# Optimization experiments

Measured on AMD Instinct MI355X. Metric: run time of the kernel, lower is better.

Reference implementation:

```python
import jax, jax.numpy as jnp
import numpy as np

EPS = 1e-12  # F.normalize default eps


def conv3d(x, w, b=None):
    # x: (B,C,D,H,W), w: (O,I,3,3,3), stride 1, padding 1 == SAME
    y = jax.lax.conv_general_dilated(
        x, w, window_strides=(1, 1, 1), padding='SAME',
        dimension_numbers=('NCDHW', 'OIDHW', 'NCDHW'))
    if b is not None:
        y = y + b[None, :, None, None, None]
    return y


def adaptive_conv(x, weights):
    # x: (B,C,D,H,W); weights: (B,27,D,H,W) per-voxel 3x3x3 kernel taps
    B, C, D, H, W = x.shape
    xp = jnp.pad(x, ((0, 0), (0, 0), (1, 1), (1, 1), (1, 1)))
    out = jnp.zeros_like(x)
    idx = 0
    for i in range(3):
        for j in range(3):
            for k in range(3):
                out = out + xp[:, :, i:i + D, j:j + H, k:k + W] * weights[:, idx][:, None]
                idx += 1
    return out


def adaptive_block(inputs, w1, b1, w2, weights_src=None):
    # weights = Conv3d(8->8) -> ReLU -> Conv3d(8->27, no bias), then L1-normalize over channel
    src = inputs if weights_src is None else weights_src
    w = conv3d(jax.nn.relu(conv3d(src, w1, b1)), w2)
    norm = jnp.maximum(jnp.sum(jnp.abs(w), axis=1, keepdims=True), EPS)
    w = w / norm
    out = inputs
    for _ in range(3):
        out = adaptive_conv(out, w)
    return out


def setup_inputs() -> dict:
    key = jax.random.key(0)
    ks = jax.random.split(key, 16)
    d = {}
    d['x'] = jax.random.normal(ks[0], (1, 8, 128, 128, 128), dtype=jnp.float32)
    s = 0.05
    d['ac1_w1'] = jax.random.normal(ks[1], (8, 8, 3, 3, 3), jnp.float32) * s
    d['ac1_b1'] = jnp.zeros((8,), jnp.float32)
    d['ac1_w2'] = jax.random.normal(ks[2], (27, 8, 3, 3, 3), jnp.float32) * s
    d['ac2_w1'] = jax.random.normal(ks[3], (8, 8, 3, 3, 3), jnp.float32) * s
    d['ac2_b1'] = jnp.zeros((8,), jnp.float32)
    d['ac2_w2'] = jax.random.normal(ks[4], (27, 8, 3, 3, 3), jnp.float32) * s
    d['ac3_w1'] = jax.random.normal(ks[5], (8, 8, 3, 3, 3), jnp.float32) * s
    d['ac3_b1'] = jnp.zeros((8,), jnp.float32)
    d['ac3_w2'] = jax.random.normal(ks[6], (27, 8, 3, 3, 3), jnp.float32) * s
    d['mid_w'] = jax.random.normal(ks[7], (8, 8, 3, 3, 3), jnp.float32) * s
    d['mid_b'] = jnp.zeros((8,), jnp.float32)
    d['out_w'] = jax.random.normal(ks[8], (1, 8, 3, 3, 3), jnp.float32) * s
    d['out_b'] = jnp.zeros((1,), jnp.float32)
    return d


def reference(x, ac1_w1, ac1_b1, ac1_w2, ac2_w1, ac2_b1, ac2_w2,
              ac3_w1, ac3_b1, ac3_w2, mid_w, mid_b, out_w, out_b):
    # Post-UNet refinement pipeline of Voxel_RefinerXL.run
    mid = adaptive_block(x, ac1_w1, ac1_b1, ac1_w2)
    mid = conv3d(mid, mid_w, mid_b)
    mid = adaptive_block(mid, ac2_w1, ac2_b1, ac2_w2)
    final = conv3d(mid, out_w, out_b)  # (B,1,D,H,W)
    final = adaptive_block(final, ac3_w1, ac3_b1, ac3_w2, weights_src=mid)
    return final
```

## Files before the change

kernel.cpp:

```cpp
#include <hip/hip_runtime.h>
#include <hip/hip_fp16.h>
#include <math.h>

#define WW 128
#define HH 128
#define DD 128
#define HW (WW * HH)
#define VOL (WW * HH * DD)
#define PW 130
#define PHW (130 * 130)
#define PVOL (130 * 130 * 130)
#define NSHELL 99848

typedef _Float16 f16x8 __attribute__((ext_vector_type(8)));
typedef _Float16 f16x4 __attribute__((ext_vector_type(4)));
typedef _Float16 f16x2 __attribute__((ext_vector_type(2)));
typedef float f32x4 __attribute__((ext_vector_type(4)));
typedef float f32x16 __attribute__((ext_vector_type(16)));
typedef int int4v __attribute__((ext_vector_type(4)));
typedef int int2v __attribute__((ext_vector_type(2)));

__device__ __forceinline__ void stv(float* p, float v) { *p = v; }
__device__ __forceinline__ void stv(_Float16* p, float v) { *p = (_Float16)v; }


template <int NCH>
__global__ __launch_bounds__(256) void zero_shell2(_Float16* __restrict__ p0,
                                                   _Float16* __restrict__ p1)
{
    _Float16* p = blockIdx.y ? p1 : p0;
    const int t = blockIdx.x * 256 + threadIdx.x;
    if (t >= NSHELL) return;
    int d, h, w;
    if (t < 33800)      { d = (t < 16900) ? 0 : 129; int r = t % 16900; h = r / 130; w = r % 130; }
    else if (t < 67080) { int r = t - 33800; h = (r < 16640) ? 0 : 129; int q = r % 16640; d = 1 + q / 130; w = q % 130; }
    else                { int r = t - 67080; w = (r < 16384) ? 0 : 129; int q = r % 16384; d = 1 + q / 128; h = 1 + q % 128; }
    const size_t site = (size_t)d * PHW + (size_t)h * PW + w;
    if (NCH == 8) *(f16x8*)(p + site * 8) = (f16x8){};
    else          p[site] = (_Float16)0.f;
}

__global__ __launch_bounds__(256) void cvt_x(const float* __restrict__ x,
                                             _Float16* __restrict__ xi)
{
    const size_t v = (size_t)blockIdx.x * 256 + threadIdx.x;
    const int d = (int)(v >> 14), h = (int)((v >> 7) & 127), w = (int)(v & 127);
    f16x8 o;
#pragma unroll
    for (int c = 0; c < 8; ++c) o[c] = (_Float16)x[(size_t)c * VOL + v];
    *(f16x8*)(xi + ((size_t)(d + 1) * PHW + (size_t)(h + 1) * PW + (w + 1)) * 8) = o;
}

__global__ __launch_bounds__(256) void prepack_all(
    const float* __restrict__ w0, const float* __restrict__ w1,
    const float* __restrict__ w2, const float* __restrict__ w3,
    const float* __restrict__ w4, const float* __restrict__ w5,
    const float* __restrict__ w6, const float* __restrict__ w7,
    _Float16* __restrict__ pb)
{
    const int b = blockIdx.x;
    const float* src; int OC; size_t off;
    switch (b) {
        case 0: src = w0; OC = 8;  off = 0;     break;
        case 1: src = w1; OC = 8;  off = 3584;  break;
        case 2: src = w2; OC = 8;  off = 7168;  break;
        case 3: src = w3; OC = 8;  off = 10752; break;
        case 4: src = w4; OC = 1;  off = 14336; break;
        case 5: src = w5; OC = 27; off = 17920; break;
        case 6: src = w6; OC = 27; off = 25088; break;
        default: src = w7; OC = 27; off = 32256; break;
    }
    const bool big = (b >= 5);
    const int total = big ? 896 : 448;
    for (int e = threadIdx.x; e < total; e += 256) {
        const int s = e >> 6, lane = e & 63;
        const int m   = big ? (lane & 31) : (lane & 15);
        const int tap = big ? (2 * s + (lane >> 5)) : (s * 4 + (lane >> 4));
        f16x8 a = {};
        if (tap < 27 && m < OC) {
#pragma unroll
            for (int j = 0; j < 8; ++j)
                a[j] = (_Float16)src[m * 216 + j * 27 + tap];
        }
        *(f16x8*)(pb + off + (size_t)e * 8) = a;
    }
}

template <int OC, bool RELU, int OM, typename TO>
__global__ __launch_bounds__(256) void conv_g(const _Float16* __restrict__ in,
                                              const _Float16* __restrict__ apack,
                                              const float* __restrict__ bias,
                                              TO* __restrict__ out)
{
    const int tid  = threadIdx.x;
    const int wid  = tid >> 6;
    const int lane = tid & 63;
    const int n    = lane & 15;
    const int quad = lane >> 4;

    const int bid = blockIdx.x;
    const int idx = bid >> 3;
    const int d   = ((bid & 7) << 4) + (idx & 15);
    const int h   = ((idx >> 4) << 2) + wid;

    f16x8 afr[7];
#pragma unroll
    for (int s = 0; s < 7; ++s)
        afr[s] = *(const f16x8*)(apack + (size_t)(s * 64 + lane) * 8);

    int voff[7];
#pragma unroll
    for (int s = 0; s < 7; ++s) {
        int tap = s * 4 + quad;
        if (tap > 26) tap = 26;
        const int kd = tap / 9, kh = (tap % 9) / 3, kw = tap % 3;
        voff[s] = (d + kd) * PHW + (h + kh) * PW + kw;
    }

    float bv[4];
#pragma unroll
    for (int r = 0; r < 4; ++r) {
        const int o = quad * 4 + r;
        bv[r] = (bias != nullptr && o < OC) ? bias[o] : 0.f;
    }

#pragma unroll 2
    for (int wseg = 0; wseg < 8; ++wseg) {
        const int wv = wseg * 16 + n;
        f16x8 bfr[7];
#pragma unroll
        for (int s = 0; s < 7; ++s)
            bfr[s] = *(const f16x8*)(in + (size_t)(voff[s] + wv) * 8);
        f32x4 acc;
        acc[0] = bv[0]; acc[1] = bv[1]; acc[2] = bv[2]; acc[3] = bv[3];
#pragma unroll
        for (int s = 0; s < 7; ++s)
            acc = __builtin_amdgcn_mfma_f32_16x16x32_f16(afr[s], bfr[s], acc, 0, 0, 0);

        if (OM == 0) {
            if (quad < 2) {
                const size_t pvox = (size_t)(d + 1) * PHW + (size_t)(h + 1) * PW + 1 + wv;
                f16x4 o4;
#pragma unroll
                for (int r = 0; r < 4; ++r) {
                    float v = acc[r];
                    if (RELU) v = fmaxf(v, 0.f);
                    o4[r] = (_Float16)v;
                }
                *(f16x4*)((_Float16*)out + pvox * 8 + quad * 4) = o4;
            }
        } else {
            if (quad == 0) {
                const size_t pvox = (size_t)(d + 1) * PHW + (size_t)(h + 1) * PW + 1 + wv;
                float v = acc[0];
                if (RELU) v = fmaxf(v, 0.f);
                stv((TO*)out + pvox, v);
            }
        }
    }
}

__global__ __launch_bounds__(256, 4) void conv27_g(const _Float16* __restrict__ in,
                                                   const _Float16* __restrict__ apack,
                                                   _Float16* __restrict__ wn)
{
    __shared__ f16x8 lds[2340];

    const int tid  = threadIdx.x;
    const int wid  = tid >> 6;
    const int lane = tid & 63;
    const int col  = lane & 31;
    const int half = lane >> 5;

    const int bid = blockIdx.x;
    const int idx = bid >> 3;
    const int d   = ((bid & 7) << 4) + (idx & 15);
    const int h0  = (idx >> 4) << 2;
    const int h   = h0 + wid;

    f16x8 sv[10];
#pragma unroll
    for (int it = 0; it < 10; ++it) {
        const int sidx = it * 256 + tid;
        if (sidx < 2340) {
            const int dd = sidx / 780;
            const int r  = sidx - dd * 780;
            const int hh = r / 130;
            const int ww = r - hh * 130;
            sv[it] = *(const f16x8*)(in + ((size_t)(d + dd) * PHW + (size_t)(h0 + hh) * PW + ww) * 8);
        }
    }
#pragma unroll
    for (int it = 0; it < 10; ++it) {
        const int sidx = it * 256 + tid;
        if (sidx < 2340) lds[sidx] = sv[it];
    }
    __syncthreads();

    f16x8 afr[14];
#pragma unroll
    for (int s = 0; s < 14; ++s)
        afr[s] = *(const f16x8*)(apack + (size_t)(s * 64 + lane) * 8);

    int vsite[14];
#pragma unroll
    for (int s = 0; s < 14; ++s) {
        int tap = 2 * s + half;
        if (tap > 26) tap = 26;
        const int kd = tap / 9, kh = (tap % 9) / 3, kw = tap % 3;
        vsite[s] = (kd * 6 + wid + kh) * 130 + kw + col;
    }

#pragma unroll 1
    for (int wseg = 0; wseg < 4; ++wseg) {
        const int wb = wseg * 32;
        f16x8 bfr[6];
#pragma unroll
        for (int s = 0; s < 6; ++s)
            bfr[s] = lds[vsite[s] + wb];
        f32x16 acc = {};
#pragma unroll
        for (int s = 0; s < 14; ++s) {
            acc = __builtin_amdgcn_mfma_f32_32x32x16_f16(afr[s], bfr[s % 6], acc, 0, 0, 0);
            if (s + 6 < 14)
                bfr[s % 6] = lds[vsite[s + 6] + wb];
        }

        float p0 = (fabsf(acc[0]) + fabsf(acc[1])) + (fabsf(acc[2]) + fabsf(acc[3]));
        float p1 = (fabsf(acc[4]) + fabsf(acc[5])) + (fabsf(acc[6]) + fabsf(acc[7]));
        float p2 = (fabsf(acc[8]) + fabsf(acc[9])) + (fabsf(acc[10]) + fabsf(acc[11]));
        float p3 = (fabsf(acc[12]) + fabsf(acc[13])) + (fabsf(acc[14]) + fabsf(acc[15]));
        float ssum = (p0 + p1) + (p2 + p3);
        ssum += __shfl_xor(ssum, 32);
        const float inv = __builtin_amdgcn_rcpf(fmaxf(ssum, 1e-12f));

        int pk[8];
#pragma unroll
        for (int i = 0; i < 8; ++i) {
            f16x2 t;
            t[0] = (_Float16)(acc[2 * i] * inv);
            t[1] = (_Float16)(acc[2 * i + 1] * inv);
            pk[i] = __builtin_bit_cast(int, t);
        }
        const size_t grp = (size_t)(d * 128 + h) * 4 + wseg;
        _Float16* gbase = wn + grp * 896;
        if (half == 0) {
            _Float16* dst = gbase + (size_t)col * 16;
            int4v v0; v0[0] = pk[0]; v0[1] = pk[1]; v0[2] = pk[2]; v0[3] = pk[3];
            int4v v1; v1[0] = pk[4]; v1[1] = pk[5]; v1[2] = pk[6]; v1[3] = pk[7];
            *(int4v*)dst = v0;
            *(int4v*)(dst + 8) = v1;
        } else {
            _Float16* dst = gbase + 512 + (size_t)col * 12;
            int2v a; a[0] = pk[0]; a[1] = pk[1];
            int2v b; b[0] = pk[2]; b[1] = pk[3];
            int2v c; c[0] = pk[4]; c[1] = pk[5];
            *(int2v*)dst = a;
            *(int2v*)(dst + 4) = b;
            *(int2v*)(dst + 8) = c;
        }
    }
}

#define WH(m) (((m) >> 2) & 1)
#define WR(m) (((m) & 3) + 4 * ((m) >> 3))

__global__ __launch_bounds__(256) void adapt8(const _Float16* __restrict__ in,
                                              const _Float16* __restrict__ wn,
                                              _Float16* __restrict__ out)
{
    const int tid = threadIdx.x;
    const int bid = blockIdx.x;
    const int d = bid >> 6;
    const int h = ((bid & 63) << 1) + (tid >> 7);
    const int w = tid & 127;
    const size_t vox = (size_t)d * HW + (size_t)h * WW + w;

    const _Float16* gb = wn + (vox >> 5) * 896;
    const int col = (int)(vox & 31);
    f16x8 wk0[2];
    wk0[0] = *(const f16x8*)(gb + (size_t)col * 16);
    wk0[1] = *(const f16x8*)(gb + (size_t)col * 16 + 8);
    f16x4 wk1[3];
    const _Float16* c1 = gb + 512 + (size_t)col * 12;
    wk1[0] = *(const f16x4*)(c1);
    wk1[1] = *(const f16x4*)(c1 + 4);
    wk1[2] = *(const f16x4*)(c1 + 8);

    float acc[8] = {0.f, 0.f, 0.f, 0.f, 0.f, 0.f, 0.f, 0.f};
#pragma unroll
    for (int kd = 0; kd < 3; ++kd) {
#pragma unroll
        for (int kh = 0; kh < 3; ++kh) {
            const _Float16* rp = in + ((size_t)(d + kd) * PHW + (size_t)(h + kh) * PW + w) * 8;
#pragma unroll
            for (int kw = 0; kw < 3; ++kw) {
                const f16x8 xv = *(const f16x8*)(rp + (size_t)kw * 8);
                const int m = kd * 9 + kh * 3 + kw;
                const int r = WR(m);
                const float wvv = WH(m) == 0 ? (float)wk0[r >> 3][r & 7]
                                             : (float)wk1[r >> 2][r & 3];
#pragma unroll
                for (int c = 0; c < 8; ++c) acc[c] += wvv * (float)xv[c];
            }
        }
    }
    f16x8 o;
#pragma unroll
    for (int c = 0; c < 8; ++c) o[c] = (_Float16)acc[c];
    *(f16x8*)(out + ((size_t)(d + 1) * PHW + (size_t)(h + 1) * PW + (w + 1)) * 8) = o;
}

template <bool PADOUT, typename TOUT>
__global__ __launch_bounds__(256) void adapt1(const _Float16* __restrict__ in,
                                              const _Float16* __restrict__ wn,
                                              TOUT* __restrict__ out)
{
    const size_t vox = (size_t)blockIdx.x * 256 + threadIdx.x;
    const int w = (int)(vox & 127);
    const int h = (int)((vox >> 7) & 127);
    const int d = (int)(vox >> 14);

    const _Float16* gb = wn + (vox >> 5) * 896;
    const int col = (int)(vox & 31);
    f16x8 wk0[2];
    wk0[0] = *(const f16x8*)(gb + (size_t)col * 16);
    wk0[1] = *(const f16x8*)(gb + (size_t)col * 16 + 8);
    f16x4 wk1[3];
    const _Float16* c1 = gb + 512 + (size_t)col * 12;
    wk1[0] = *(const f16x4*)(c1);
    wk1[1] = *(const f16x4*)(c1 + 4);
    wk1[2] = *(const f16x4*)(c1 + 8);

    float acc = 0.f;
#pragma unroll
    for (int kd = 0; kd < 3; ++kd) {
#pragma unroll
        for (int kh = 0; kh < 3; ++kh) {
            const _Float16* rp = in + (size_t)(d + kd) * PHW + (size_t)(h + kh) * PW + w;
#pragma unroll
            for (int kw = 0; kw < 3; ++kw) {
                const int m = kd * 9 + kh * 3 + kw;
                const int r = WR(m);
                const float wvv = WH(m) == 0 ? (float)wk0[r >> 3][r & 7]
                                             : (float)wk1[r >> 2][r & 3];
                acc += wvv * (float)rp[kw];
            }
        }
    }
    if (PADOUT)
        stv(out + (size_t)(d + 1) * PHW + (size_t)(h + 1) * PW + (w + 1), acc);
    else
        stv(out + vox, acc);
}

extern "C" void kernel_launch(void* const* d_in, const int* in_sizes, int n_in,
                              void* d_out, int out_size, void* d_ws, size_t ws_size,
                              hipStream_t stream)
{
    (void)in_sizes; (void)n_in; (void)out_size; (void)ws_size;

    const float* x      = (const float*)d_in[0];
    const float* ac1_w1 = (const float*)d_in[1];
    const float* ac1_b1 = (const float*)d_in[2];
    const float* ac1_w2 = (const float*)d_in[3];
    const float* ac2_w1 = (const float*)d_in[4];
    const float* ac2_b1 = (const float*)d_in[5];
    const float* ac2_w2 = (const float*)d_in[6];
    const float* ac3_w1 = (const float*)d_in[7];
    const float* ac3_b1 = (const float*)d_in[8];
    const float* ac3_w2 = (const float*)d_in[9];
    const float* mid_w  = (const float*)d_in[10];
    const float* mid_b  = (const float*)d_in[11];
    const float* out_w  = (const float*)d_in[12];
    const float* out_b  = (const float*)d_in[13];
    float* outp = (float*)d_out;

    const size_t V = (size_t)VOL;
    _Float16* Wb  = (_Float16*)d_ws;
    _Float16* B1i = Wb + 32 * V;
    _Float16* B2i = B1i + (size_t)8 * PVOL;
    _Float16* F0  = B2i + (size_t)8 * PVOL;
    _Float16* F1  = F0 + (size_t)PVOL;
    _Float16* PB  = F1 + (size_t)PVOL;

    _Float16* pk_ac1w1 = PB + 0;
    _Float16* pk_ac2w1 = PB + 3584;
    _Float16* pk_ac3w1 = PB + 7168;
    _Float16* pk_midw  = PB + 10752;
    _Float16* pk_outw  = PB + 14336;
    _Float16* pk_ac1w2 = PB + 17920;
    _Float16* pk_ac2w2 = PB + 25088;
    _Float16* pk_ac3w2 = PB + 32256;

    const dim3 cgrid(4096), cblk(256);
    const dim3 a8grid(8192), a8blk(256);
    const dim3 a1grid(8192), a1blk(256);
    const dim3 zgrid((NSHELL + 255) / 256, 2), zblk(256);

    zero_shell2<8><<<zgrid, zblk, 0, stream>>>(B1i, B2i);
    zero_shell2<1><<<zgrid, zblk, 0, stream>>>(F0, F1);
    prepack_all<<<8, 256, 0, stream>>>(ac1_w1, ac2_w1, ac3_w1, mid_w, out_w,
                                       ac1_w2, ac2_w2, ac3_w2, PB);
    cvt_x<<<8192, 256, 0, stream>>>(x, B2i);

    conv_g<8, true, 0, _Float16><<<cgrid, cblk, 0, stream>>>(B2i, pk_ac1w1, ac1_b1, B1i);
    conv27_g<<<cgrid, cblk, 0, stream>>>(B1i, pk_ac1w2, Wb);
    adapt8<<<a8grid, a8blk, 0, stream>>>(B2i, Wb, B1i);
    adapt8<<<a8grid, a8blk, 0, stream>>>(B1i, Wb, B2i);
    adapt8<<<a8grid, a8blk, 0, stream>>>(B2i, Wb, B1i);
    conv_g<8, false, 0, _Float16><<<cgrid, cblk, 0, stream>>>(B1i, pk_midw, mid_b, B2i);

    conv_g<8, true, 0, _Float16><<<cgrid, cblk, 0, stream>>>(B2i, pk_ac2w1, ac2_b1, B1i);
    conv27_g<<<cgrid, cblk, 0, stream>>>(B1i, pk_ac2w2, Wb);
    adapt8<<<a8grid, a8blk, 0, stream>>>(B2i, Wb, B1i);
    adapt8<<<a8grid, a8blk, 0, stream>>>(B1i, Wb, B2i);
    adapt8<<<a8grid, a8blk, 0, stream>>>(B2i, Wb, B1i);

    conv_g<8, true, 0, _Float16><<<cgrid, cblk, 0, stream>>>(B1i, pk_ac3w1, ac3_b1, B2i);
    conv27_g<<<cgrid, cblk, 0, stream>>>(B2i, pk_ac3w2, Wb);
    conv_g<1, false, 2, _Float16><<<cgrid, cblk, 0, stream>>>(B1i, pk_outw, out_b, F0);
    adapt1<true, _Float16><<<a1grid, a1blk, 0, stream>>>(F0, Wb, F1);
    adapt1<true, _Float16><<<a1grid, a1blk, 0, stream>>>(F1, Wb, F0);
    adapt1<false, float><<<a1grid, a1blk, 0, stream>>>(F0, Wb, outp);
}
```

Measured before the change: 734.9 us.

## Stage adaptive-conv input halo tiles in LDS with 4-row blocks

The adapt8 and adapt1 kernels now use 512-thread blocks covering a 4-row by 128-wide strip of one depth slice. Each block cooperatively loads its 3x6x130 padded input halo into shared memory, then reads the 27 neighbour taps from LDS instead of issuing 27 global loads per voxel. This targets redundant global/L2 traffic from overlapping stencil reads. In exchange it adds a barrier, integer divisions in the load phase, and LDS use (about 37 KB for adapt8) that may limit occupancy.

```diff
diff --git a/kernel.cpp b/kernel.cpp
--- a/kernel.cpp
+++ b/kernel.cpp
@@ -265,17 +265,38 @@
 #define WH(m) (((m) >> 2) & 1)
 #define WR(m) (((m) & 3) + 4 * ((m) >> 3))
 
-__global__ __launch_bounds__(256) void adapt8(const _Float16* __restrict__ in,
+__global__ __launch_bounds__(512) void adapt8(const _Float16* __restrict__ in,
                                               const _Float16* __restrict__ wn,
                                               _Float16* __restrict__ out)
 {
+    __shared__ f16x8 lds[2340];
+
     const int tid = threadIdx.x;
     const int bid = blockIdx.x;
-    const int d = bid >> 6;
-    const int h = ((bid & 63) << 1) + (tid >> 7);
-    const int w = tid & 127;
+    const int d  = bid >> 5;
+    const int h0 = (bid & 31) << 2;
+    const int hl = tid >> 7;
+    const int w  = tid & 127;
+    const int h  = h0 + hl;
+
+    f16x8 sv[5];
+#pragma unroll
+    for (int it = 0; it < 5; ++it) {
+        const int s = it * 512 + tid;
+        if (s < 2340) {
+            const int dd = s / 780, r = s - dd * 780;
+            const int hh = r / 130, ww = r - hh * 130;
+            sv[it] = *(const f16x8*)(in + ((size_t)(d + dd) * PHW + (size_t)(h0 + hh) * PW + ww) * 8);
+        }
+    }
+#pragma unroll
+    for (int it = 0; it < 5; ++it) {
+        const int s = it * 512 + tid;
+        if (s < 2340) lds[s] = sv[it];
+    }
+    __syncthreads();
+
     const size_t vox = (size_t)d * HW + (size_t)h * WW + w;
-
     const _Float16* gb = wn + (vox >> 5) * 896;
     const int col = (int)(vox & 31);
     f16x8 wk0[2];
@@ -292,10 +313,10 @@
     for (int kd = 0; kd < 3; ++kd) {
 #pragma unroll
         for (int kh = 0; kh < 3; ++kh) {
-            const _Float16* rp = in + ((size_t)(d + kd) * PHW + (size_t)(h + kh) * PW + w) * 8;
+            const int rowb = (kd * 6 + hl + kh) * 130 + w;
 #pragma unroll
             for (int kw = 0; kw < 3; ++kw) {
-                const f16x8 xv = *(const f16x8*)(rp + (size_t)kw * 8);
+                const f16x8 xv = lds[rowb + kw];
                 const int m = kd * 9 + kh * 3 + kw;
                 const int r = WR(m);
                 const float wvv = WH(m) == 0 ? (float)wk0[r >> 3][r & 7]
@@ -312,15 +333,38 @@
 }
 
 template <bool PADOUT, typename TOUT>
-__global__ __launch_bounds__(256) void adapt1(const _Float16* __restrict__ in,
+__global__ __launch_bounds__(512) void adapt1(const _Float16* __restrict__ in,
                                               const _Float16* __restrict__ wn,
                                               TOUT* __restrict__ out)
 {
-    const size_t vox = (size_t)blockIdx.x * 256 + threadIdx.x;
-    const int w = (int)(vox & 127);
-    const int h = (int)((vox >> 7) & 127);
-    const int d = (int)(vox >> 14);
-
+    __shared__ _Float16 lds1[2340];
+
+    const int tid = threadIdx.x;
+    const int bid = blockIdx.x;
+    const int d  = bid >> 5;
+    const int h0 = (bid & 31) << 2;
+    const int hl = tid >> 7;
+    const int w  = tid & 127;
+    const int h  = h0 + hl;
+
+    _Float16 sv[5];
+#pragma unroll
+    for (int it = 0; it < 5; ++it) {
+        const int s = it * 512 + tid;
+        if (s < 2340) {
+            const int dd = s / 780, r = s - dd * 780;
+            const int hh = r / 130, ww = r - hh * 130;
+            sv[it] = in[(size_t)(d + dd) * PHW + (size_t)(h0 + hh) * PW + ww];
+        }
+    }
+#pragma unroll
+    for (int it = 0; it < 5; ++it) {
+        const int s = it * 512 + tid;
+        if (s < 2340) lds1[s] = sv[it];
+    }
+    __syncthreads();
+
+    const size_t vox = (size_t)d * HW + (size_t)h * WW + w;
     const _Float16* gb = wn + (vox >> 5) * 896;
     const int col = (int)(vox & 31);
     f16x8 wk0[2];
@@ -337,14 +381,14 @@
     for (int kd = 0; kd < 3; ++kd) {
 #pragma unroll
         for (int kh = 0; kh < 3; ++kh) {
-            const _Float16* rp = in + (size_t)(d + kd) * PHW + (size_t)(h + kh) * PW + w;
+            const int rowb = (kd * 6 + hl + kh) * 130 + w;
 #pragma unroll
             for (int kw = 0; kw < 3; ++kw) {
                 const int m = kd * 9 + kh * 3 + kw;
                 const int r = WR(m);
                 const float wvv = WH(m) == 0 ? (float)wk0[r >> 3][r & 7]
                                              : (float)wk1[r >> 2][r & 3];
-                acc += wvv * (float)rp[kw];
+                acc += wvv * (float)lds1[rowb + kw];
             }
         }
     }
@@ -394,8 +438,8 @@
     _Float16* pk_ac3w2 = PB + 32256;
 
     const dim3 cgrid(4096), cblk(256);
-    const dim3 a8grid(8192), a8blk(256);
-    const dim3 a1grid(8192), a1blk(256);
+    const dim3 a8grid(4096), a8blk(512);
+    const dim3 a1grid(4096), a1blk(512);
     const dim3 zgrid((NSHELL + 255) / 256, 2), zblk(256);
 
     zero_shell2<8><<<zgrid, zblk, 0, stream>>>(B1i, B2i);
```

Measured after the change: 736.0 us. About the same (+0.1%).
